# Kernel optimization log

Hardware: AMD Instinct MI355X
Metric: run time of the kernel (lower is better)

Reference implementation:

```python
import jax, jax.numpy as jnp
import numpy as np

HD = 64        # hidden_dim
H = 4          # heads
N = 50000      # nodes
E = 400000     # edges (before self loops)
NEG_ATT = 0.2  # GATConv attention LeakyReLU slope (PyG default)
NEG_ACT = 0.01 # nn.LeakyReLU() default slope
EPS = 1e-5     # BatchNorm eps


def _bn(x, gamma, beta):
    # training-mode BatchNorm1d over node dimension (biased variance)
    mu = x.mean(0)
    var = x.var(0)
    return gamma * (x - mu) * jax.lax.rsqrt(var + EPS) + beta


def _gatconv(h_in, src, dst, W, a_src, a_dst, bias, heads, outc, concat):
    n = h_in.shape[0]
    h = (h_in @ W.T).reshape(n, heads, outc)              # [N,H,C]
    al_s = jnp.einsum('nhc,hc->nh', h, a_src)             # [N,H]
    al_d = jnp.einsum('nhc,hc->nh', h, a_dst)
    e = jax.nn.leaky_relu(al_s[src] + al_d[dst], NEG_ATT) # [E',H]
    # softmax over incoming edges of each destination node
    m = jax.lax.stop_gradient(jax.ops.segment_max(e, dst, num_segments=n))
    ex = jnp.exp(e - m[dst])
    den = jax.ops.segment_sum(ex, dst, num_segments=n)
    alpha = ex / den[dst]                                  # [E',H]
    out = jax.ops.segment_sum(h[src] * alpha[..., None], dst, num_segments=n)
    out = out.reshape(n, heads * outc) if concat else out.mean(axis=1)
    return out + bias


def setup_inputs() -> dict:
    ks = jax.random.split(jax.random.key(0), 20)
    s = 0.1
    d = {
        'x': jax.random.normal(ks[0], (N, 2 * HD), jnp.float32),
        'edge_index': jax.random.randint(ks[1], (2, E), 0, N, jnp.int64),
        'W1': jax.random.normal(ks[2], (H * HD, 2 * HD), jnp.float32) * s,
        'a1s': jax.random.normal(ks[3], (H, HD), jnp.float32) * s,
        'a1d': jax.random.normal(ks[4], (H, HD), jnp.float32) * s,
        'b1': jnp.zeros((H * HD,), jnp.float32),
        'W2': jax.random.normal(ks[5], (H * HD, H * HD), jnp.float32) * s,
        'a2s': jax.random.normal(ks[6], (H, HD), jnp.float32) * s,
        'a2d': jax.random.normal(ks[7], (H, HD), jnp.float32) * s,
        'b2': jnp.zeros((H * HD,), jnp.float32),
        'W3': jax.random.normal(ks[8], (1 * HD, H * HD), jnp.float32) * s,
        'a3s': jax.random.normal(ks[9], (1, HD), jnp.float32) * s,
        'a3d': jax.random.normal(ks[10], (1, HD), jnp.float32) * s,
        'b3': jnp.zeros((HD,), jnp.float32),
        'gamma': jnp.ones((H * HD,), jnp.float32),
        'beta': jnp.zeros((H * HD,), jnp.float32),
    }
    return d


def reference(x, edge_index, W1, a1s, a1d, b1, W2, a2s, a2d, b2,
              W3, a3s, a3d, b3, gamma, beta):
    n = x.shape[0]
    loop = jnp.arange(n, dtype=edge_index.dtype)
    src = jnp.concatenate([edge_index[0], loop])  # add_self_loops=True
    dst = jnp.concatenate([edge_index[1], loop])

    h = _gatconv(x, src, dst, W1, a1s, a1d, b1, H, HD, True)
    h = jax.nn.leaky_relu(_bn(h, gamma, beta), NEG_ACT)

    # single middle residual block (num_layers=3); dropout is identity (eval)
    res = h
    h = _gatconv(h, src, dst, W2, a2s, a2d, b2, H, HD, True)
    h = jax.nn.leaky_relu(_bn(h, gamma, beta), NEG_ACT)
    h = h + res

    out = _gatconv(h, src, dst, W3, a3s, a3d, b3, 1, HD, False)
    return out
```

## Files before the change

### kernel.cpp

```cpp
#include <hip/hip_runtime.h>
#include <hip/hip_bf16.h>

#define NEG_ATT 0.2f
#define NEG_ACT 0.01f

typedef __attribute__((ext_vector_type(8))) short short8;
typedef __attribute__((ext_vector_type(4))) float f32x4;

__device__ __forceinline__ unsigned short f2bf(float f) {
    unsigned int u = __float_as_uint(f);
    unsigned int r = (u + 0x7fff + ((u >> 16) & 1)) >> 16;
    return (unsigned short)r;
}
__device__ __forceinline__ float b2f(unsigned short h) {
    return __uint_as_float((unsigned int)h << 16);
}


__global__ void init_deg(int* deg, int Nn) {
    int t = blockIdx.x * 256 + threadIdx.x;
    if (t < Nn) deg[t] = 1;
}

__global__ void count_edges(const int* __restrict__ ei, int* deg, int E) {
    int t = blockIdx.x * 256 + threadIdx.x;
    if (t < E) atomicAdd(&deg[ei[E + t]], 1);
}

#define SCAN_CHUNK 1024
__global__ void scan1(const int* __restrict__ deg, int* __restrict__ offs,
                      int* blocksum, int Nn) {
    __shared__ int sh[256];
    int b = blockIdx.x, t = threadIdx.x;
    int base = b * SCAN_CHUNK + t * 4;
    int v[4];
    int s = 0;
    for (int j = 0; j < 4; j++) {
        int idx = base + j;
        v[j] = (idx < Nn) ? deg[idx] : 0;
        s += v[j];
    }
    sh[t] = s;
    __syncthreads();
    for (int off = 1; off < 256; off <<= 1) {
        int x = (t >= off) ? sh[t - off] : 0;
        __syncthreads();
        sh[t] += x;
        __syncthreads();
    }
    int excl = sh[t] - s;
    if (t == 255) blocksum[b] = sh[255];
    int run = excl;
    for (int j = 0; j < 4; j++) {
        int idx = base + j;
        if (idx < Nn) offs[idx] = run;
        run += v[j];
    }
}

__global__ void scan23(int* __restrict__ offs, const int* __restrict__ bsum,
                       int* __restrict__ cursor, int Nn, int G) {
    int i = blockIdx.x * 256 + threadIdx.x;
    if (i > Nn) return;
    int g = i >> 10;
    int basev = 0;
    for (int k = 0; k < g; k++) basev += bsum[k];
    if (i == Nn) {
        int tot = basev;
        for (int k = g; k < G; k++) tot += bsum[k];
        offs[Nn] = tot;
        return;
    }
    int v = offs[i] + basev;
    offs[i] = v;
    cursor[i] = v;
}

__global__ void fill_csr(const int* __restrict__ ei, int* cursor, int* csr, int E, int Nn) {
    int t = blockIdx.x * 256 + threadIdx.x;
    if (t < E) {
        int s = ei[t];
        int d = ei[E + t];
        int p = atomicAdd(&cursor[d], 1);
        csr[p] = s;
    } else if (t < E + Nn) {
        int nn = t - E;
        int p = atomicAdd(&cursor[nn], 1);
        csr[p] = nn;
    }
}


__global__ __launch_bounds__(256) void f2b_all(
    const float* __restrict__ x, unsigned short* __restrict__ xb, int nx, int nxpad,
    const float* __restrict__ w1, unsigned short* __restrict__ o1, int n1,
    const float* __restrict__ w2, unsigned short* __restrict__ o2, int n2,
    const float* __restrict__ w3, unsigned short* __restrict__ o3, int n3) {
    int i = (blockIdx.x * 256 + threadIdx.x) * 8;
    const float* in;
    unsigned short* out;
    if (i < nxpad) {
        if (i >= nx) {
            *(ushort4*)&xb[i] = make_ushort4(0, 0, 0, 0);
            *(ushort4*)&xb[i + 4] = make_ushort4(0, 0, 0, 0);
            return;
        }
        in = x + i; out = xb + i;
    } else {
        int j = i - nxpad;
        if (j < n1) { in = w1 + j; out = o1 + j; }
        else if (j < n1 + n2) { in = w2 + (j - n1); out = o2 + (j - n1); }
        else if (j < n1 + n2 + n3) { in = w3 + (j - n1 - n2); out = o3 + (j - n1 - n2); }
        else return;
    }
    float4 a = *(const float4*)in;
    float4 b = *(const float4*)(in + 4);
    *(ushort4*)out = make_ushort4(f2bf(a.x), f2bf(a.y), f2bf(a.z), f2bf(a.w));
    *(ushort4*)(out + 4) = make_ushort4(f2bf(b.x), f2bf(b.y), f2bf(b.z), f2bf(b.w));
}


template <int K, int CO, int HEADS>
__global__ __launch_bounds__(256) void gemm_mfma(
    const unsigned short* __restrict__ Xb, const unsigned short* __restrict__ Wb,
    unsigned short* __restrict__ Hb, const float* __restrict__ a_s,
    const float* __restrict__ a_d, float* __restrict__ als, float* __restrict__ ald) {
    constexpr int BM = 128, BN = 64, BK = 64, LD = 72, SLD = 68;
    __shared__ __align__(16) char smem[4 * 32 * SLD * 4];
    unsigned short* As = (unsigned short*)smem;
    unsigned short* Bs = As + BM * LD;
    int tid = threadIdx.x;
    int wave = tid >> 6, lane = tid & 63;
    int quad = lane >> 4, l16 = lane & 15;
    int m0 = blockIdx.x * BM, n0 = blockIdx.y * BN;
    int hd = blockIdx.y;
    int arow = tid >> 3;
    int achk = (tid & 7) * 8;
    f32x4 acc[2][4] = {};
    for (int k0 = 0; k0 < K; k0 += BK) {
        __syncthreads();
#pragma unroll
        for (int p = 0; p < 4; p++) {
            int r = arow + p * 32;
            *(int4*)&As[r * LD + achk] = *(const int4*)&Xb[(size_t)(m0 + r) * K + k0 + achk];
        }
#pragma unroll
        for (int p = 0; p < 2; p++) {
            int r = arow + p * 32;
            *(int4*)&Bs[r * LD + achk] = *(const int4*)&Wb[(size_t)(n0 + r) * K + k0 + achk];
        }
        __syncthreads();
#pragma unroll
        for (int ks = 0; ks < 2; ks++) {
            short8 af[2], bfr[4];
#pragma unroll
            for (int i = 0; i < 2; i++)
                af[i] = *(const short8*)&As[(wave * 32 + i * 16 + l16) * LD + ks * 32 + quad * 8];
#pragma unroll
            for (int j = 0; j < 4; j++)
                bfr[j] = *(const short8*)&Bs[(j * 16 + l16) * LD + ks * 32 + quad * 8];
#pragma unroll
            for (int i = 0; i < 2; i++)
#pragma unroll
                for (int j = 0; j < 4; j++)
                    acc[i][j] = __builtin_amdgcn_mfma_f32_16x16x32_bf16(af[i], bfr[j], acc[i][j], 0, 0, 0);
        }
    }
    __syncthreads();

    float asv[4], adv[4];
#pragma unroll
    for (int j = 0; j < 4; j++) {
        asv[j] = a_s[hd * 64 + j * 16 + l16];
        adv[j] = a_d[hd * 64 + j * 16 + l16];
    }
#pragma unroll
    for (int i = 0; i < 2; i++)
#pragma unroll
        for (int r = 0; r < 4; r++) {
            float ps = acc[i][0][r] * asv[0] + acc[i][1][r] * asv[1] +
                       acc[i][2][r] * asv[2] + acc[i][3][r] * asv[3];
            float pd = acc[i][0][r] * adv[0] + acc[i][1][r] * adv[1] +
                       acc[i][2][r] * adv[2] + acc[i][3][r] * adv[3];
#pragma unroll
            for (int mm = 1; mm < 16; mm <<= 1) {
                ps += __shfl_xor(ps, mm);
                pd += __shfl_xor(pd, mm);
            }
            if (l16 == 0) {
                int m = m0 + wave * 32 + i * 16 + quad * 4 + r;
                als[m * HEADS + hd] = ps;
                ald[m * HEADS + hd] = pd;
            }
        }

    float* stg = (float*)smem + wave * 32 * SLD;
#pragma unroll
    for (int i = 0; i < 2; i++)
#pragma unroll
        for (int j = 0; j < 4; j++)
#pragma unroll
            for (int r = 0; r < 4; r++)
                stg[(i * 16 + quad * 4 + r) * SLD + j * 16 + l16] = acc[i][j][r];
    int g = lane >> 3, c8 = (lane & 7) * 8;
#pragma unroll
    for (int p = 0; p < 4; p++) {
        int row = p * 8 + g;
        float4 v0 = *(const float4*)&stg[row * SLD + c8];
        float4 v1 = *(const float4*)&stg[row * SLD + c8 + 4];
        uint4 o;
        o.x = ((unsigned)f2bf(v0.y) << 16) | f2bf(v0.x);
        o.y = ((unsigned)f2bf(v0.w) << 16) | f2bf(v0.z);
        o.z = ((unsigned)f2bf(v1.y) << 16) | f2bf(v1.x);
        o.w = ((unsigned)f2bf(v1.w) << 16) | f2bf(v1.z);
        *(uint4*)&Hb[(size_t)(m0 + wave * 32 + row) * CO + n0 + c8] = o;
    }
}


__global__ __launch_bounds__(256) void aggregate_h4(
    const unsigned short* __restrict__ Hb, const float* __restrict__ als,
    const float* __restrict__ ald, const int* __restrict__ offs,
    const int* __restrict__ csr, const float* __restrict__ bias,
    float* __restrict__ Yout, int Nn) {
    int wave = threadIdx.x >> 6;
    int lane = threadIdx.x & 63;
    int n = blockIdx.x * 4 + wave;
    if (n >= Nn) return;
    int hd = lane >> 4;
    int c4 = lane * 4;
    float aldn = ald[n * 4 + hd];
    int beg = offs[n], end = offs[n + 1];
    float4 acc = make_float4(0.f, 0.f, 0.f, 0.f);
    float den = 0.f;
    for (int b = beg; b < end; b += 64) {
        int cnt = min(64, end - b);
        int idx = 0;
        if (lane < cnt) idx = csr[b + lane];
        int j = 0;
        for (; j + 4 <= cnt; j += 4) {
            int s0 = __shfl(idx, j), s1 = __shfl(idx, j + 1);
            int s2 = __shfl(idx, j + 2), s3 = __shfl(idx, j + 3);
            float a0 = als[s0 * 4 + hd];
            float a1 = als[s1 * 4 + hd];
            float a2 = als[s2 * 4 + hd];
            float a3 = als[s3 * 4 + hd];
            ushort4 h0 = *(const ushort4*)&Hb[(size_t)s0 * 256 + c4];
            ushort4 h1 = *(const ushort4*)&Hb[(size_t)s1 * 256 + c4];
            ushort4 h2 = *(const ushort4*)&Hb[(size_t)s2 * 256 + c4];
            ushort4 h3 = *(const ushort4*)&Hb[(size_t)s3 * 256 + c4];
            float e0 = a0 + aldn; e0 = e0 > 0.f ? e0 : NEG_ATT * e0;
            float e1 = a1 + aldn; e1 = e1 > 0.f ? e1 : NEG_ATT * e1;
            float e2 = a2 + aldn; e2 = e2 > 0.f ? e2 : NEG_ATT * e2;
            float e3 = a3 + aldn; e3 = e3 > 0.f ? e3 : NEG_ATT * e3;
            float w0 = __expf(e0), w1 = __expf(e1), w2 = __expf(e2), w3 = __expf(e3);
            den += (w0 + w1) + (w2 + w3);
            acc.x += w0 * b2f(h0.x) + w1 * b2f(h1.x) + w2 * b2f(h2.x) + w3 * b2f(h3.x);
            acc.y += w0 * b2f(h0.y) + w1 * b2f(h1.y) + w2 * b2f(h2.y) + w3 * b2f(h3.y);
            acc.z += w0 * b2f(h0.z) + w1 * b2f(h1.z) + w2 * b2f(h2.z) + w3 * b2f(h3.z);
            acc.w += w0 * b2f(h0.w) + w1 * b2f(h1.w) + w2 * b2f(h2.w) + w3 * b2f(h3.w);
        }
        for (; j < cnt; j++) {
            int s = __shfl(idx, j);
            float e = als[s * 4 + hd] + aldn;
            e = e > 0.f ? e : NEG_ATT * e;
            float w = __expf(e);
            den += w;
            ushort4 hv = *(const ushort4*)&Hb[(size_t)s * 256 + c4];
            acc.x += w * b2f(hv.x); acc.y += w * b2f(hv.y);
            acc.z += w * b2f(hv.z); acc.w += w * b2f(hv.w);
        }
    }
    float inv = 1.f / den;
    float4 bv = *(const float4*)&bias[c4];
    float4 o = make_float4(acc.x * inv + bv.x, acc.y * inv + bv.y,
                           acc.z * inv + bv.z, acc.w * inv + bv.w);
    *(float4*)&Yout[(size_t)n * 256 + c4] = o;
}

__global__ __launch_bounds__(256) void aggregate_h1(
    const unsigned short* __restrict__ Hb, const float* __restrict__ als,
    const float* __restrict__ ald, const int* __restrict__ offs,
    const int* __restrict__ csr, const float* __restrict__ bias,
    float* __restrict__ Yout, int Nn) {
    int wave = threadIdx.x >> 6;
    int lane = threadIdx.x & 63;
    int sub = lane >> 4, lane16 = lane & 15;
    int n = blockIdx.x * 16 + wave * 4 + sub;
    if (n >= Nn) return;
    int c4 = lane16 * 4;
    float aldn = ald[n];
    int beg = offs[n], end = offs[n + 1];
    float4 acc = make_float4(0.f, 0.f, 0.f, 0.f);
    float den = 0.f;
    for (int b = beg; b < end; b += 16) {
        int cnt = min(16, end - b);
        int idx = 0;
        if (lane16 < cnt) idx = csr[b + lane16];
        int j = 0;
        for (; j + 4 <= cnt; j += 4) {
            int s0 = __shfl(idx, (sub << 4) + j);
            int s1 = __shfl(idx, (sub << 4) + j + 1);
            int s2 = __shfl(idx, (sub << 4) + j + 2);
            int s3 = __shfl(idx, (sub << 4) + j + 3);
            float a0 = als[s0], a1 = als[s1], a2 = als[s2], a3 = als[s3];
            ushort4 h0 = *(const ushort4*)&Hb[(size_t)s0 * 64 + c4];
            ushort4 h1 = *(const ushort4*)&Hb[(size_t)s1 * 64 + c4];
            ushort4 h2 = *(const ushort4*)&Hb[(size_t)s2 * 64 + c4];
            ushort4 h3 = *(const ushort4*)&Hb[(size_t)s3 * 64 + c4];
            float e0 = a0 + aldn; e0 = e0 > 0.f ? e0 : NEG_ATT * e0;
            float e1 = a1 + aldn; e1 = e1 > 0.f ? e1 : NEG_ATT * e1;
            float e2 = a2 + aldn; e2 = e2 > 0.f ? e2 : NEG_ATT * e2;
            float e3 = a3 + aldn; e3 = e3 > 0.f ? e3 : NEG_ATT * e3;
            float w0 = __expf(e0), w1 = __expf(e1), w2 = __expf(e2), w3 = __expf(e3);
            den += (w0 + w1) + (w2 + w3);
            acc.x += w0 * b2f(h0.x) + w1 * b2f(h1.x) + w2 * b2f(h2.x) + w3 * b2f(h3.x);
            acc.y += w0 * b2f(h0.y) + w1 * b2f(h1.y) + w2 * b2f(h2.y) + w3 * b2f(h3.y);
            acc.z += w0 * b2f(h0.z) + w1 * b2f(h1.z) + w2 * b2f(h2.z) + w3 * b2f(h3.z);
            acc.w += w0 * b2f(h0.w) + w1 * b2f(h1.w) + w2 * b2f(h2.w) + w3 * b2f(h3.w);
        }
        for (; j < cnt; j++) {
            int s = __shfl(idx, (sub << 4) + j);
            float e = als[s] + aldn;
            e = e > 0.f ? e : NEG_ATT * e;
            float w = __expf(e);
            den += w;
            ushort4 hv = *(const ushort4*)&Hb[(size_t)s * 64 + c4];
            acc.x += w * b2f(hv.x); acc.y += w * b2f(hv.y);
            acc.z += w * b2f(hv.z); acc.w += w * b2f(hv.w);
        }
    }
    float inv = 1.f / den;
    float4 bv = *(const float4*)&bias[c4];
    float4 o = make_float4(acc.x * inv + bv.x, acc.y * inv + bv.y,
                           acc.z * inv + bv.z, acc.w * inv + bv.w);
    *(float4*)&Yout[(size_t)n * 64 + c4] = o;
}


__global__ __launch_bounds__(256) void bn_stats(const float* __restrict__ Y,
                                                float* __restrict__ partial, int Nn) {
    __shared__ float red[4 * 512];
    int t = threadIdx.x;
    int g = blockIdx.x;
    int rows_per = (Nn + gridDim.x - 1) / gridDim.x;
    int r0 = g * rows_per;
    int r1 = min(r0 + rows_per, Nn);
    int sub = t >> 6;
    int c4 = (t & 63) * 4;
    float4 s = make_float4(0.f, 0.f, 0.f, 0.f);
    float4 q = make_float4(0.f, 0.f, 0.f, 0.f);
    for (int r = r0 + sub; r < r1; r += 4) {
        float4 v = *(const float4*)&Y[(size_t)r * 256 + c4];
        s.x += v.x; s.y += v.y; s.z += v.z; s.w += v.w;
        q.x += v.x * v.x; q.y += v.y * v.y; q.z += v.z * v.z; q.w += v.w * v.w;
    }
    float* rs = &red[sub * 512];
    rs[c4 + 0] = s.x; rs[c4 + 1] = s.y; rs[c4 + 2] = s.z; rs[c4 + 3] = s.w;
    rs[256 + c4 + 0] = q.x; rs[256 + c4 + 1] = q.y;
    rs[256 + c4 + 2] = q.z; rs[256 + c4 + 3] = q.w;
    __syncthreads();
    float v0 = red[t] + red[512 + t] + red[1024 + t] + red[1536 + t];
    float v1 = red[256 + t] + red[768 + t] + red[1280 + t] + red[1792 + t];
    partial[(size_t)g * 512 + t] = v0;
    partial[(size_t)g * 512 + 256 + t] = v1;
}

__global__ __launch_bounds__(256) void bn_reduce_final(
    const float* __restrict__ partial, int NP, const float* __restrict__ gamma,
    const float* __restrict__ beta, float* scale, float* shift, int Nn) {
    __shared__ float sh[8];
    int ch = blockIdx.x;
    int t = threadIdx.x;
    int wave = t >> 6, lane = t & 63;
    float s = 0.f, q = 0.f;
    for (int i = t; i < NP; i += 256) {
        s += partial[(size_t)i * 512 + ch];
        q += partial[(size_t)i * 512 + 256 + ch];
    }
    for (int off = 32; off; off >>= 1) {
        s += __shfl_down(s, off);
        q += __shfl_down(q, off);
    }
    if (lane == 0) { sh[wave] = s; sh[4 + wave] = q; }
    __syncthreads();
    if (t == 0) {
        s = sh[0] + sh[1] + sh[2] + sh[3];
        q = sh[4] + sh[5] + sh[6] + sh[7];
        float inv_n = 1.f / (float)Nn;
        float mu = s * inv_n;
        float var = q * inv_n - mu * mu;
        float sc = gamma[ch] * rsqrtf(var + 1e-5f);
        scale[ch] = sc;
        shift[ch] = beta[ch] - mu * sc;
    }
}

template <bool RES>
__global__ __launch_bounds__(256) void bn_apply(const float* __restrict__ Y,
                                                const float* __restrict__ scale,
                                                const float* __restrict__ shift,
                                                unsigned short* __restrict__ OutB,
                                                int total4, int total4pad) {
    int i = blockIdx.x * 256 + threadIdx.x;
    if (i >= total4pad) return;
    if (i >= total4) {
        *(ushort4*)&OutB[i * 4] = make_ushort4(0, 0, 0, 0);
        return;
    }
    float4 v = ((const float4*)Y)[i];
    int cb = (i * 4) & 255;
    float4 sc = *(const float4*)&scale[cb];
    float4 sh = *(const float4*)&shift[cb];
    float4 o;
    o.x = sc.x * v.x + sh.x; o.x = o.x > 0.f ? o.x : NEG_ACT * o.x;
    o.y = sc.y * v.y + sh.y; o.y = o.y > 0.f ? o.y : NEG_ACT * o.y;
    o.z = sc.z * v.z + sh.z; o.z = o.z > 0.f ? o.z : NEG_ACT * o.z;
    o.w = sc.w * v.w + sh.w; o.w = o.w > 0.f ? o.w : NEG_ACT * o.w;
    if (RES) {
        ushort4 r = *(const ushort4*)&OutB[i * 4];
        o.x += b2f(r.x); o.y += b2f(r.y); o.z += b2f(r.z); o.w += b2f(r.w);
    }
    *(ushort4*)&OutB[i * 4] = make_ushort4(f2bf(o.x), f2bf(o.y), f2bf(o.z), f2bf(o.w));
}


extern "C" void kernel_launch(void* const* d_in, const int* in_sizes, int n_in,
                              void* d_out, int out_size, void* d_ws, size_t ws_size,
                              hipStream_t stream) {
    const float* x    = (const float*)d_in[0];
    const int*   ei   = (const int*)d_in[1];
    const float* W1   = (const float*)d_in[2];
    const float* a1s  = (const float*)d_in[3];
    const float* a1d  = (const float*)d_in[4];
    const float* b1   = (const float*)d_in[5];
    const float* W2   = (const float*)d_in[6];
    const float* a2s  = (const float*)d_in[7];
    const float* a2d  = (const float*)d_in[8];
    const float* b2   = (const float*)d_in[9];
    const float* W3   = (const float*)d_in[10];
    const float* a3s  = (const float*)d_in[11];
    const float* a3d  = (const float*)d_in[12];
    const float* b3   = (const float*)d_in[13];
    const float* gamma = (const float*)d_in[14];
    const float* beta  = (const float*)d_in[15];
    float* out = (float*)d_out;

    const int Nn = in_sizes[0] / 128;
    const int E  = in_sizes[1] / 2;
    const int Ep = E + Nn;
    const int Mpad = (Nn + 127) & ~127;

    size_t off = 0;
    char* base = (char*)d_ws;
    auto alloc = [&](size_t bytes) -> void* {
        void* p = base + off;
        off = (off + bytes + 255) & ~(size_t)255;
        return p;
    };
    unsigned short* Hb   = (unsigned short*)alloc((size_t)Mpad * 256 * 2);
    float* bufB   = (float*)alloc((size_t)Nn * 256 * 4);
    unsigned short* xb1  = (unsigned short*)alloc((size_t)Mpad * 128 * 2);
    unsigned short* xbig = (unsigned short*)alloc((size_t)Mpad * 256 * 2);
    unsigned short* wb1  = (unsigned short*)alloc((size_t)256 * 128 * 2);
    unsigned short* wb2  = (unsigned short*)alloc((size_t)256 * 256 * 2);
    unsigned short* wb3  = (unsigned short*)alloc((size_t)64 * 256 * 2);
    float* als    = (float*)alloc((size_t)Mpad * 4 * 4);
    float* ald    = (float*)alloc((size_t)Mpad * 4 * 4);
    int*   deg    = (int*)alloc((size_t)Nn * 4);
    int*   offs   = (int*)alloc((size_t)(Nn + 1) * 4);
    int*   cursor = (int*)alloc((size_t)Nn * 4);
    int*   bsum   = (int*)alloc(64 * 4);
    int*   csr    = (int*)alloc((size_t)Ep * 4);
    const int NP = 1024;
    float* partial = (float*)alloc((size_t)NP * 512 * 4);
    float* scale  = (float*)alloc(256 * 4);
    float* shift  = (float*)alloc(256 * 4);
    (void)ws_size;

    const int G = (Nn + SCAN_CHUNK - 1) / SCAN_CHUNK;

    init_deg<<<(Nn + 255) / 256, 256, 0, stream>>>(deg, Nn);
    count_edges<<<(E + 255) / 256, 256, 0, stream>>>(ei, deg, E);
    scan1<<<G, 256, 0, stream>>>(deg, offs, bsum, Nn);
    scan23<<<(Nn + 1 + 255) / 256, 256, 0, stream>>>(offs, bsum, cursor, Nn, G);
    fill_csr<<<(Ep + 255) / 256, 256, 0, stream>>>(ei, cursor, csr, E, Nn);

    {
        int nxpad = Mpad * 128;
        int wtot = 256 * 128 + 256 * 256 + 64 * 256;
        f2b_all<<<((nxpad + wtot) / 8 + 255) / 256, 256, 0, stream>>>(
            x, xb1, Nn * 128, nxpad, W1, wb1, 256 * 128, W2, wb2, 256 * 256, W3, wb3, 64 * 256);
    }

    const int gm = Mpad / 128;
    const int nagg4 = (Nn + 3) / 4;
    const int nagg1 = (Nn + 15) / 16;
    const int total4 = Nn * 64;
    const int total4pad = Mpad * 64;
    const int napply = (total4pad + 255) / 256;

    gemm_mfma<128, 256, 4><<<dim3(gm, 4), 256, 0, stream>>>(xb1, wb1, Hb, a1s, a1d, als, ald);
    aggregate_h4<<<nagg4, 256, 0, stream>>>(Hb, als, ald, offs, csr, b1, bufB, Nn);
    bn_stats<<<NP, 256, 0, stream>>>(bufB, partial, Nn);
    bn_reduce_final<<<256, 256, 0, stream>>>(partial, NP, gamma, beta, scale, shift, Nn);
    bn_apply<false><<<napply, 256, 0, stream>>>(bufB, scale, shift, xbig, total4, total4pad);

    gemm_mfma<256, 256, 4><<<dim3(gm, 4), 256, 0, stream>>>(xbig, wb2, Hb, a2s, a2d, als, ald);
    aggregate_h4<<<nagg4, 256, 0, stream>>>(Hb, als, ald, offs, csr, b2, bufB, Nn);
    bn_stats<<<NP, 256, 0, stream>>>(bufB, partial, Nn);
    bn_reduce_final<<<256, 256, 0, stream>>>(partial, NP, gamma, beta, scale, shift, Nn);
    bn_apply<true><<<napply, 256, 0, stream>>>(bufB, scale, shift, xbig, total4, total4pad);

    gemm_mfma<256, 64, 1><<<dim3(gm, 1), 256, 0, stream>>>(xbig, wb3, Hb, a3s, a3d, als, ald);
    aggregate_h1<<<nagg1, 256, 0, stream>>>(Hb, als, ald, offs, csr, b3, out, Nn);
}
```

Before: 363.0 us.

## Store aggregation output in bf16, drop pre-BN bias, fuse degree init, unroll gather

Aggregation now writes bf16 instead of fp32 and omits the bias, which training-mode BatchNorm cancels. BN stats and apply read the bf16 buffer, halving traffic on the largest intermediate. Degree initialisation is folded into the fp32-to-bf16 conversion kernel to save a launch, and the edge gather loop is unrolled by 8 for more loads in flight. Rounding the pre-BN activations to bf16 adds precision loss.

```diff
diff --git a/kernel.cpp b/kernel.cpp
--- a/kernel.cpp
+++ b/kernel.cpp
@@ -16,11 +16,6 @@
     return __uint_as_float((unsigned int)h << 16);
 }
 
-
-__global__ void init_deg(int* deg, int Nn) {
-    int t = blockIdx.x * 256 + threadIdx.x;
-    if (t < Nn) deg[t] = 1;
-}
 
 __global__ void count_edges(const int* __restrict__ ei, int* deg, int E) {
     int t = blockIdx.x * 256 + threadIdx.x;
@@ -91,12 +86,21 @@
 }
 
 
-__global__ __launch_bounds__(256) void f2b_all(
+__global__ __launch_bounds__(256) void prep_all(
+    int* __restrict__ deg, int Nn,
     const float* __restrict__ x, unsigned short* __restrict__ xb, int nx, int nxpad,
     const float* __restrict__ w1, unsigned short* __restrict__ o1, int n1,
     const float* __restrict__ w2, unsigned short* __restrict__ o2, int n2,
     const float* __restrict__ w3, unsigned short* __restrict__ o3, int n3) {
-    int i = (blockIdx.x * 256 + threadIdx.x) * 8;
+    int id = blockIdx.x * 256 + threadIdx.x;
+    int nconv = (nxpad + n1 + n2 + n3) / 8;
+    if (id >= nconv) {
+        int d0 = (id - nconv) * 8;
+        for (int k = 0; k < 8; k++)
+            if (d0 + k < Nn) deg[d0 + k] = 1;
+        return;
+    }
+    int i = id * 8;
     const float* in;
     unsigned short* out;
     if (i < nxpad) {
@@ -110,8 +114,7 @@
         int j = i - nxpad;
         if (j < n1) { in = w1 + j; out = o1 + j; }
         else if (j < n1 + n2) { in = w2 + (j - n1); out = o2 + (j - n1); }
-        else if (j < n1 + n2 + n3) { in = w3 + (j - n1 - n2); out = o3 + (j - n1 - n2); }
-        else return;
+        else { in = w3 + (j - n1 - n2); out = o3 + (j - n1 - n2); }
     }
     float4 a = *(const float4*)in;
     float4 b = *(const float4*)(in + 4);
@@ -218,11 +221,30 @@
 }
 
 
+#define EDGE4(sA, sB, sC, sD)                                                        \
+    {                                                                                \
+        float a0 = als[(sA)*4 + hd], a1 = als[(sB)*4 + hd];                          \
+        float a2 = als[(sC)*4 + hd], a3 = als[(sD)*4 + hd];                          \
+        ushort4 h0 = *(const ushort4*)&Hb[(size_t)(sA)*256 + c4];                    \
+        ushort4 h1 = *(const ushort4*)&Hb[(size_t)(sB)*256 + c4];                    \
+        ushort4 h2 = *(const ushort4*)&Hb[(size_t)(sC)*256 + c4];                    \
+        ushort4 h3 = *(const ushort4*)&Hb[(size_t)(sD)*256 + c4];                    \
+        float e0 = a0 + aldn; e0 = e0 > 0.f ? e0 : NEG_ATT * e0;                     \
+        float e1 = a1 + aldn; e1 = e1 > 0.f ? e1 : NEG_ATT * e1;                     \
+        float e2 = a2 + aldn; e2 = e2 > 0.f ? e2 : NEG_ATT * e2;                     \
+        float e3 = a3 + aldn; e3 = e3 > 0.f ? e3 : NEG_ATT * e3;                     \
+        float w0 = __expf(e0), w1 = __expf(e1), w2 = __expf(e2), w3 = __expf(e3);    \
+        den += (w0 + w1) + (w2 + w3);                                                \
+        acc.x += w0 * b2f(h0.x) + w1 * b2f(h1.x) + w2 * b2f(h2.x) + w3 * b2f(h3.x);  \
+        acc.y += w0 * b2f(h0.y) + w1 * b2f(h1.y) + w2 * b2f(h2.y) + w3 * b2f(h3.y);  \
+        acc.z += w0 * b2f(h0.z) + w1 * b2f(h1.z) + w2 * b2f(h2.z) + w3 * b2f(h3.z);  \
+        acc.w += w0 * b2f(h0.w) + w1 * b2f(h1.w) + w2 * b2f(h2.w) + w3 * b2f(h3.w);  \
+    }
+
 __global__ __launch_bounds__(256) void aggregate_h4(
     const unsigned short* __restrict__ Hb, const float* __restrict__ als,
     const float* __restrict__ ald, const int* __restrict__ offs,
-    const int* __restrict__ csr, const float* __restrict__ bias,
-    float* __restrict__ Yout, int Nn) {
+    const int* __restrict__ csr, unsigned short* __restrict__ Yb, int Nn) {
     int wave = threadIdx.x >> 6;
     int lane = threadIdx.x & 63;
     int n = blockIdx.x * 4 + wave;
@@ -238,27 +260,18 @@
         int idx = 0;
         if (lane < cnt) idx = csr[b + lane];
         int j = 0;
+        for (; j + 8 <= cnt; j += 8) {
+            int s0 = __shfl(idx, j), s1 = __shfl(idx, j + 1);
+            int s2 = __shfl(idx, j + 2), s3 = __shfl(idx, j + 3);
+            int s4 = __shfl(idx, j + 4), s5 = __shfl(idx, j + 5);
+            int s6 = __shfl(idx, j + 6), s7 = __shfl(idx, j + 7);
+            EDGE4(s0, s1, s2, s3);
+            EDGE4(s4, s5, s6, s7);
+        }
         for (; j + 4 <= cnt; j += 4) {
             int s0 = __shfl(idx, j), s1 = __shfl(idx, j + 1);
             int s2 = __shfl(idx, j + 2), s3 = __shfl(idx, j + 3);
-            float a0 = als[s0 * 4 + hd];
-            float a1 = als[s1 * 4 + hd];
-            float a2 = als[s2 * 4 + hd];
-            float a3 = als[s3 * 4 + hd];
-            ushort4 h0 = *(const ushort4*)&Hb[(size_t)s0 * 256 + c4];
-            ushort4 h1 = *(const ushort4*)&Hb[(size_t)s1 * 256 + c4];
-            ushort4 h2 = *(const ushort4*)&Hb[(size_t)s2 * 256 + c4];
-            ushort4 h3 = *(const ushort4*)&Hb[(size_t)s3 * 256 + c4];
-            float e0 = a0 + aldn; e0 = e0 > 0.f ? e0 : NEG_ATT * e0;
-            float e1 = a1 + aldn; e1 = e1 > 0.f ? e1 : NEG_ATT * e1;
-            float e2 = a2 + aldn; e2 = e2 > 0.f ? e2 : NEG_ATT * e2;
-            float e3 = a3 + aldn; e3 = e3 > 0.f ? e3 : NEG_ATT * e3;
-            float w0 = __expf(e0), w1 = __expf(e1), w2 = __expf(e2), w3 = __expf(e3);
-            den += (w0 + w1) + (w2 + w3);
-            acc.x += w0 * b2f(h0.x) + w1 * b2f(h1.x) + w2 * b2f(h2.x) + w3 * b2f(h3.x);
-            acc.y += w0 * b2f(h0.y) + w1 * b2f(h1.y) + w2 * b2f(h2.y) + w3 * b2f(h3.y);
-            acc.z += w0 * b2f(h0.z) + w1 * b2f(h1.z) + w2 * b2f(h2.z) + w3 * b2f(h3.z);
-            acc.w += w0 * b2f(h0.w) + w1 * b2f(h1.w) + w2 * b2f(h2.w) + w3 * b2f(h3.w);
+            EDGE4(s0, s1, s2, s3);
         }
         for (; j < cnt; j++) {
             int s = __shfl(idx, j);
@@ -272,10 +285,8 @@
         }
     }
     float inv = 1.f / den;
-    float4 bv = *(const float4*)&bias[c4];
-    float4 o = make_float4(acc.x * inv + bv.x, acc.y * inv + bv.y,
-                           acc.z * inv + bv.z, acc.w * inv + bv.w);
-    *(float4*)&Yout[(size_t)n * 256 + c4] = o;
+    *(ushort4*)&Yb[(size_t)n * 256 + c4] = make_ushort4(
+        f2bf(acc.x * inv), f2bf(acc.y * inv), f2bf(acc.z * inv), f2bf(acc.w * inv));
 }
 
 __global__ __launch_bounds__(256) void aggregate_h1(
@@ -338,7 +349,7 @@
 }
 
 
-__global__ __launch_bounds__(256) void bn_stats(const float* __restrict__ Y,
+__global__ __launch_bounds__(256) void bn_stats(const unsigned short* __restrict__ Yb,
                                                 float* __restrict__ partial, int Nn) {
     __shared__ float red[4 * 512];
     int t = threadIdx.x;
@@ -351,9 +362,10 @@
     float4 s = make_float4(0.f, 0.f, 0.f, 0.f);
     float4 q = make_float4(0.f, 0.f, 0.f, 0.f);
     for (int r = r0 + sub; r < r1; r += 4) {
-        float4 v = *(const float4*)&Y[(size_t)r * 256 + c4];
-        s.x += v.x; s.y += v.y; s.z += v.z; s.w += v.w;
-        q.x += v.x * v.x; q.y += v.y * v.y; q.z += v.z * v.z; q.w += v.w * v.w;
+        ushort4 u = *(const ushort4*)&Yb[(size_t)r * 256 + c4];
+        float vx = b2f(u.x), vy = b2f(u.y), vz = b2f(u.z), vw = b2f(u.w);
+        s.x += vx; s.y += vy; s.z += vz; s.w += vw;
+        q.x += vx * vx; q.y += vy * vy; q.z += vz * vz; q.w += vw * vw;
     }
     float* rs = &red[sub * 512];
     rs[c4 + 0] = s.x; rs[c4 + 1] = s.y; rs[c4 + 2] = s.z; rs[c4 + 3] = s.w;
@@ -397,7 +409,7 @@
 }
 
 template <bool RES>
-__global__ __launch_bounds__(256) void bn_apply(const float* __restrict__ Y,
+__global__ __launch_bounds__(256) void bn_apply(const unsigned short* __restrict__ Yb,
                                                 const float* __restrict__ scale,
                                                 const float* __restrict__ shift,
                                                 unsigned short* __restrict__ OutB,
@@ -408,15 +420,15 @@
         *(ushort4*)&OutB[i * 4] = make_ushort4(0, 0, 0, 0);
         return;
     }
-    float4 v = ((const float4*)Y)[i];
+    ushort4 u = *(const ushort4*)&Yb[i * 4];
     int cb = (i * 4) & 255;
     float4 sc = *(const float4*)&scale[cb];
     float4 sh = *(const float4*)&shift[cb];
     float4 o;
-    o.x = sc.x * v.x + sh.x; o.x = o.x > 0.f ? o.x : NEG_ACT * o.x;
-    o.y = sc.y * v.y + sh.y; o.y = o.y > 0.f ? o.y : NEG_ACT * o.y;
-    o.z = sc.z * v.z + sh.z; o.z = o.z > 0.f ? o.z : NEG_ACT * o.z;
-    o.w = sc.w * v.w + sh.w; o.w = o.w > 0.f ? o.w : NEG_ACT * o.w;
+    o.x = sc.x * b2f(u.x) + sh.x; o.x = o.x > 0.f ? o.x : NEG_ACT * o.x;
+    o.y = sc.y * b2f(u.y) + sh.y; o.y = o.y > 0.f ? o.y : NEG_ACT * o.y;
+    o.z = sc.z * b2f(u.z) + sh.z; o.z = o.z > 0.f ? o.z : NEG_ACT * o.z;
+    o.w = sc.w * b2f(u.w) + sh.w; o.w = o.w > 0.f ? o.w : NEG_ACT * o.w;
     if (RES) {
         ushort4 r = *(const ushort4*)&OutB[i * 4];
         o.x += b2f(r.x); o.y += b2f(r.y); o.z += b2f(r.z); o.w += b2f(r.w);
@@ -433,11 +445,9 @@
     const float* W1   = (const float*)d_in[2];
     const float* a1s  = (const float*)d_in[3];
     const float* a1d  = (const float*)d_in[4];
-    const float* b1   = (const float*)d_in[5];
     const float* W2   = (const float*)d_in[6];
     const float* a2s  = (const float*)d_in[7];
     const float* a2d  = (const float*)d_in[8];
-    const float* b2   = (const float*)d_in[9];
     const float* W3   = (const float*)d_in[10];
     const float* a3s  = (const float*)d_in[11];
     const float* a3d  = (const float*)d_in[12];
@@ -459,7 +469,7 @@
         return p;
     };
     unsigned short* Hb   = (unsigned short*)alloc((size_t)Mpad * 256 * 2);
-    float* bufB   = (float*)alloc((size_t)Nn * 256 * 4);
+    unsigned short* Yb   = (unsigned short*)alloc((size_t)Nn * 256 * 2);
     unsigned short* xb1  = (unsigned short*)alloc((size_t)Mpad * 128 * 2);
     unsigned short* xbig = (unsigned short*)alloc((size_t)Mpad * 256 * 2);
     unsigned short* wb1  = (unsigned short*)alloc((size_t)256 * 128 * 2);
@@ -480,18 +490,20 @@
 
     const int G = (Nn + SCAN_CHUNK - 1) / SCAN_CHUNK;
 
-    init_deg<<<(Nn + 255) / 256, 256, 0, stream>>>(deg, Nn);
+    {
+        int nxpad = Mpad * 128;
+        int wtot = 256 * 128 + 256 * 256 + 64 * 256;
+        int nconv = (nxpad + wtot) / 8;
+        int ndeg = (Nn + 7) / 8;
+        prep_all<<<(nconv + ndeg + 255) / 256, 256, 0, stream>>>(
+            deg, Nn, x, xb1, Nn * 128, nxpad,
+            W1, wb1, 256 * 128, W2, wb2, 256 * 256, W3, wb3, 64 * 256);
+    }
+
     count_edges<<<(E + 255) / 256, 256, 0, stream>>>(ei, deg, E);
     scan1<<<G, 256, 0, stream>>>(deg, offs, bsum, Nn);
     scan23<<<(Nn + 1 + 255) / 256, 256, 0, stream>>>(offs, bsum, cursor, Nn, G);
     fill_csr<<<(Ep + 255) / 256, 256, 0, stream>>>(ei, cursor, csr, E, Nn);
-
-    {
-        int nxpad = Mpad * 128;
-        int wtot = 256 * 128 + 256 * 256 + 64 * 256;
-        f2b_all<<<((nxpad + wtot) / 8 + 255) / 256, 256, 0, stream>>>(
-            x, xb1, Nn * 128, nxpad, W1, wb1, 256 * 128, W2, wb2, 256 * 256, W3, wb3, 64 * 256);
-    }
 
     const int gm = Mpad / 128;
     const int nagg4 = (Nn + 3) / 4;
@@ -501,16 +513,16 @@
     const int napply = (total4pad + 255) / 256;
 
     gemm_mfma<128, 256, 4><<<dim3(gm, 4), 256, 0, stream>>>(xb1, wb1, Hb, a1s, a1d, als, ald);
-    aggregate_h4<<<nagg4, 256, 0, stream>>>(Hb, als, ald, offs, csr, b1, bufB, Nn);
-    bn_stats<<<NP, 256, 0, stream>>>(bufB, partial, Nn);
+    aggregate_h4<<<nagg4, 256, 0, stream>>>(Hb, als, ald, offs, csr, Yb, Nn);
+    bn_stats<<<NP, 256, 0, stream>>>(Yb, partial, Nn);
     bn_reduce_final<<<256, 256, 0, stream>>>(partial, NP, gamma, beta, scale, shift, Nn);
-    bn_apply<false><<<napply, 256, 0, stream>>>(bufB, scale, shift, xbig, total4, total4pad);
+    bn_apply<false><<<napply, 256, 0, stream>>>(Yb, scale, shift, xbig, total4, total4pad);
 
     gemm_mfma<256, 256, 4><<<dim3(gm, 4), 256, 0, stream>>>(xbig, wb2, Hb, a2s, a2d, als, ald);
-    aggregate_h4<<<nagg4, 256, 0, stream>>>(Hb, als, ald, offs, csr, b2, bufB, Nn);
-    bn_stats<<<NP, 256, 0, stream>>>(bufB, partial, Nn);
+    aggregate_h4<<<nagg4, 256, 0, stream>>>(Hb, als, ald, offs, csr, Yb, Nn);
+    bn_stats<<<NP, 256, 0, stream>>>(Yb, partial, Nn);
     bn_reduce_final<<<256, 256, 0, stream>>>(partial, NP, gamma, beta, scale, shift, Nn);
-    bn_apply<true><<<napply, 256, 0, stream>>>(bufB, scale, shift, xbig, total4, total4pad);
+    bn_apply<true><<<napply, 256, 0, stream>>>(Yb, scale, shift, xbig, total4, total4pad);
 
     gemm_mfma<256, 64, 1><<<dim3(gm, 1), 256, 0, stream>>>(xbig, wb3, Hb, a3s, a3d, als, ald);
     aggregate_h1<<<nagg1, 256, 0, stream>>>(Hb, als, ald, offs, csr, b3, out, Nn);
```

Result: faster. 339.5 us (-6.5%).
